# Kernel tuning notes

Hardware: AMD Instinct MI355X
Metric: run time of the kernel (lower is better)

Reference implementation:

```python
import jax, jax.numpy as jnp
import numpy as np

LMAX, MMAX = 4, 2
C_IN, C_OUT = 128, 128           # sphere_channels, m_output_channels
NUM_EXPERTS = 8
NUM_SYSTEMS = 16
NUM_EDGES = 12288
M_SIZE = [LMAX + 1, 2 * (LMAX - 1 + 1), 2 * (LMAX - 2 + 1)]  # [5, 8, 6]


def _mole_linear(x, W, ce, b=None):
    """MoLE linear: per-edge expert mixing of weights, equivalently mixing of
    per-expert outputs.  x: [N, in] or [N, 2, in]; W: [K, in, out]; ce: [N, K]."""
    if x.ndim == 2:
        z = jnp.einsum('ni,kio->nko', x, W)        # [N, K, out]
        y = jnp.einsum('nk,nko->no', ce, z)
    else:
        z = jnp.einsum('nci,kio->nkco', x, W)      # [N, K, 2, out]
        y = jnp.einsum('nk,nkco->nco', ce, z)
    if b is not None:
        y = y + ce @ b                              # mixed bias, b: [K, out]
    return y


def setup_inputs() -> dict:
    key = jax.random.key(0)
    ks = jax.random.split(key, 8)
    num_mcoef = sum(M_SIZE)  # 19
    x = jax.random.normal(ks[0], (NUM_EDGES, num_mcoef, C_IN), dtype=jnp.float32)
    x_edge = jax.random.normal(ks[1], (NUM_EDGES, C_IN), dtype=jnp.float32)
    expert_coefficients = jax.random.uniform(ks[2], (NUM_SYSTEMS, NUM_EXPERTS), dtype=jnp.float32)
    edge_batch = jax.random.randint(ks[3], (NUM_EDGES,), 0, NUM_SYSTEMS)
    # fc_m0: in = (lmax+1)*C, out = (lmax+1)*C_out, with bias
    in0 = (LMAX + 1) * C_IN
    out0 = (LMAX + 1) * C_OUT
    W_m0 = jax.random.normal(ks[4], (NUM_EXPERTS, in0, out0), dtype=jnp.float32) * 0.02
    b_m0 = jnp.zeros((NUM_EXPERTS, out0), dtype=jnp.float32)
    # so2_m_conv m: in = (lmax-m+1)*C, out = 2*(lmax-m+1)*C_out, no bias
    nc1 = LMAX - 1 + 1
    W_m1 = jax.random.normal(ks[5], (NUM_EXPERTS, nc1 * C_IN, 2 * nc1 * C_OUT), dtype=jnp.float32) * 0.02
    nc2 = LMAX - 2 + 1
    W_m2 = jax.random.normal(ks[6], (NUM_EXPERTS, nc2 * C_IN, 2 * nc2 * C_OUT), dtype=jnp.float32) * 0.02
    return {
        'x': x, 'x_edge': x_edge,
        'expert_coefficients': expert_coefficients, 'edge_batch': edge_batch,
        'W_m0': W_m0, 'b_m0': b_m0, 'W_m1': W_m1, 'W_m2': W_m2,
    }


def reference(x, x_edge, expert_coefficients, edge_batch, W_m0, b_m0, W_m1, W_m2):
    N = x.shape[0]
    ce = expert_coefficients[edge_batch]               # [N, K] per-edge mix coeffs
    x0, x1, x2 = jnp.split(x, np.cumsum(M_SIZE[:-1]), axis=1)
    # m = 0 branch (internal_weights=True -> no radial rescale)
    y0 = _mole_linear(x0.reshape(N, -1), W_m0, ce, b_m0)
    out = [y0.reshape(N, -1, C_OUT)]                   # [N, lmax+1, C_out]
    # m >= 1 branches: SO(2) real/imag recombination
    for m, Wm, xm in ((1, W_m1, x1), (2, W_m2, x2)):
        nc = LMAX - m + 1
        xm = xm.reshape(N, 2, nc * C_IN)
        ym = _mole_linear(xm, Wm, ce)                  # [N, 2, 2*nc*C_out]
        ym = ym.reshape(N, 4, nc * C_OUT)
        x_m_r = ym[:, 0] - ym[:, 3]                    # x_r_0 - x_i_1
        x_m_i = ym[:, 2] + ym[:, 1]                    # x_r_1 + x_i_0
        out.append(x_m_r.reshape(N, nc, C_OUT))
        out.append(x_m_i.reshape(N, nc, C_OUT))
    return jnp.concatenate(out, axis=1)                # [N, 19, C_out]
```

## Files before the change

kernel.cpp:

```cpp
#include <hip/hip_runtime.h>
#include <cstdint>

#define N_EDGES 12288
#define ROWLEN  2432
#define CAP     2048

typedef __bf16 bf16;
typedef __bf16 bf16x8 __attribute__((ext_vector_type(8)));
typedef float  f32x4  __attribute__((ext_vector_type(4)));

#define ELEMS0 (640*640)
#define ELEMS1 (1024*1024)
#define ELEMS2 (768*768)

#define WS_IDX_OFF   1024
#define WS_BIAS_OFF  (WS_IDX_OFF + 16*CAP*4)
#define WS_W_OFF     (WS_BIAS_OFF + 16*640*4)
#define WZ_ELEMS     ((size_t)16*(ELEMS0+ELEMS1+ELEMS2))

template<int B> struct Cfg;
template<> struct Cfg<0> { static constexpr int K=640,  KS=640, XOFF=0,    NT=5;
                           static constexpr size_t WOFF=0; };
template<> struct Cfg<1> { static constexpr int K=1024, KS=512, XOFF=640,  NT=8;
                           static constexpr size_t WOFF=(size_t)16*ELEMS0; };
template<> struct Cfg<2> { static constexpr int K=768,  KS=384, XOFF=1664, NT=6;
                           static constexpr size_t WOFF=(size_t)16*ELEMS0+(size_t)16*ELEMS1; };

__device__ __forceinline__ void async_copy16(const void* g, void* l) {
  auto gp = reinterpret_cast<const __attribute__((address_space(1))) unsigned int*>(
      reinterpret_cast<uintptr_t>(g));
  auto lp = reinterpret_cast<__attribute__((address_space(3))) unsigned int*>(
      (unsigned int)reinterpret_cast<uintptr_t>(l));
  __builtin_amdgcn_global_load_lds(gp, lp, 16, 0, 0);
}

__global__ void bucket_kernel(const int* __restrict__ eb, int* __restrict__ counts,
                              int* __restrict__ idxb) {
  __shared__ int hcnt[16], hbase[16];
  int tid = threadIdx.x;
  int t = blockIdx.x * 256 + tid;
  if (tid < 16) hcnt[tid] = 0;
  __syncthreads();
  int s = -1, lp = 0;
  if (t < N_EDGES) { s = eb[t]; lp = atomicAdd(&hcnt[s], 1); }
  __syncthreads();
  if (tid < 16) hbase[tid] = atomicAdd(counts + tid, hcnt[tid]);
  __syncthreads();
  if (s >= 0) { int p = hbase[s] + lp; if (p < CAP) idxb[s * CAP + p] = t; }
}

__global__ void bias_kernel(const float* __restrict__ ce, const float* __restrict__ b0,
                            float* __restrict__ bias) {
  int t = blockIdx.x * 256 + threadIdx.x;
  int s = t / 640, c = t - s * 640;
  float a = 0.f;
#pragma unroll
  for (int e = 0; e < 8; ++e) a += ce[s * 8 + e] * b0[e * 640 + c];
  bias[t] = a;
}

template<int B>
__device__ __forceinline__ void mix_body(const float* __restrict__ Wsrc,
                                         const float* ce_s,
                                         unsigned short* __restrict__ Wz, int pos) {
  constexpr int N = Cfg<B>::K, KS = Cfg<B>::KS, NT = N / 128, HALF = N / 2;
  constexpr int SRC_STRIDE = KS * N;
  constexpr size_t DST_STRIDE = (size_t)Cfg<B>::K * N;
  int nn = pos & 127, kgrp = (pos >> 7) & 3, rest = pos >> 9;
  int nt = rest % NT, kblk = rest / NT;
  int i0 = kblk * 32 + kgrp * 8;
  int c  = nt * 128 + nn;
  int si = i0, sc = c; float sg = 1.f;
  if (B > 0 && i0 >= KS) {
    si = i0 - KS;
    if (c < HALF) { sc = c + HALF; sg = -1.f; } else { sc = c - HALF; }
  }
  float w[8][8];
  const float* p0 = Wsrc + (size_t)si * N + sc;
#pragma unroll
  for (int e = 0; e < 8; ++e) {
    const float* p = p0 + (size_t)e * SRC_STRIDE;
#pragma unroll
    for (int j = 0; j < 8; ++j)
      w[e][j] = sg * __builtin_nontemporal_load(p + (size_t)j * N);
  }
  unsigned short* db = Wz + Cfg<B>::WOFF + (size_t)pos * 8;
#pragma unroll
  for (int s = 0; s < 16; ++s) {
    float a[8] = {0, 0, 0, 0, 0, 0, 0, 0};
#pragma unroll
    for (int e = 0; e < 8; ++e) {
      float cc = ce_s[s * 8 + e];
#pragma unroll
      for (int j = 0; j < 8; ++j) a[j] += cc * w[e][j];
    }
    bf16x8 v;
#pragma unroll
    for (int j = 0; j < 8; ++j) v[j] = (bf16)a[j];
    *(bf16x8*)(db + s * DST_STRIDE) = v;
  }
}

__global__ __launch_bounds__(256) void mix_all(const float* __restrict__ W0,
                                               const float* __restrict__ W1,
                                               const float* __restrict__ W2,
                                               const float* __restrict__ ce,
                                               unsigned short* __restrict__ Wz) {
  __shared__ float ce_s[128];
  int tid = threadIdx.x;
  if (tid < 128) ce_s[tid] = ce[tid];
  __syncthreads();
  int bx = blockIdx.x;
  if (bx < 200)      mix_body<0>(W0, ce_s, Wz, bx * 256 + tid);
  else if (bx < 712) mix_body<1>(W1, ce_s, Wz, (bx - 200) * 256 + tid);
  else               mix_body<2>(W2, ce_s, Wz, (bx - 712) * 256 + tid);
}

template<int B>
__device__ __forceinline__ void gemm_body(
    const float* __restrict__ x, const char* __restrict__ zeros,
    const unsigned short* __restrict__ Wz,
    const int* __restrict__ counts, const int* __restrict__ idxb,
    const float* __restrict__ bias, float* __restrict__ out,
    int s, int mt, int nt2, char* sm, int* eidx)
{
  constexpr int K = Cfg<B>::K, NT = Cfg<B>::NT, KB = K / 32, XOFF = Cfg<B>::XOFF;
  int cnt = counts[s];
  int m0 = mt * 128;
  if (m0 >= cnt) return;
  int tid = threadIdx.x;
  if (tid < 128) eidx[tid] = (m0 + tid < cnt) ? idxb[s * CAP + m0 + tid] : -1;
  __syncthreads();
  char* lA0 = sm;           char* lA1 = sm + 8192;
  char* lB0 = sm + 16384;   char* lB1 = sm + 32768;
  int wv = tid >> 6, ln = tid & 63;
  int wm = wv >> 1, wn = wv & 1;
  int kq = ln >> 4, lm = ln & 15;
  int c0 = nt2 * 2;
  int r_a = tid >> 1, h = tid & 1;
  const char* arow; int kinc;
  { int e = eidx[r_a];
    if (e >= 0) { arow = (const char*)(x + (size_t)e * ROWLEN + XOFF); kinc = 128; }
    else        { arow = zeros; kinc = 0; } }
  const unsigned short* wb = Wz + Cfg<B>::WOFF + (size_t)s * K * K;

  f32x4 sreg[4];
  auto loadA = [&](int kb) {
    const char* p = arow + (size_t)kb * kinc + h * 64;
#pragma unroll
    for (int i = 0; i < 4; ++i) sreg[i] = *(const f32x4*)(p + i * 16);
  };
  auto writeA = [&](char* dst) {
#pragma unroll
    for (int c = 0; c < 2; ++c) {
      bf16x8 v;
#pragma unroll
      for (int j = 0; j < 8; ++j) v[j] = (bf16)sreg[c * 2 + (j >> 2)][j & 3];
      *(bf16x8*)(dst + ((2 * h + c) * 128 + r_a) * 16) = v;
    }
  };
  auto stageB = [&](int kb, char* dst) {
    const unsigned short* base = wb + (size_t)kb * (NT * 4096);
#pragma unroll
    for (int i = 0; i < 4; ++i) {
      int c = i * 256 + tid;
      int ck = c0 + (c >> 9); if (ck > NT - 1) ck = NT - 1;
      async_copy16(base + (size_t)ck * 4096 + (c & 511) * 8,
                   dst + (i * 256 + wv * 64) * 16);
    }
  };

  f32x4 acc[4][8];
#pragma unroll
  for (int i = 0; i < 4; ++i)
#pragma unroll
    for (int j = 0; j < 8; ++j) {
      acc[i][j][0] = 0.f; acc[i][j][1] = 0.f; acc[i][j][2] = 0.f; acc[i][j][3] = 0.f;
    }

  loadA(0); stageB(0, lB0); writeA(lA0);
#pragma unroll 1
  for (int kb = 0; kb < KB; ++kb) {
    __syncthreads();
    char* la = (kb & 1) ? lA1 : lA0;
    char* lb = (kb & 1) ? lB1 : lB0;
    if (kb + 1 < KB) {
      loadA(kb + 1);
      stageB(kb + 1, (kb & 1) ? lB0 : lB1);
    }
    bf16x8 af[4], bq[8];
#pragma unroll
    for (int mi = 0; mi < 4; ++mi)
      af[mi] = *(const bf16x8*)(la + kq * 2048 + (wm * 64 + mi * 16 + lm) * 16);
#pragma unroll
    for (int ni = 0; ni < 8; ++ni)
      bq[ni] = *(const bf16x8*)(lb + wn * 8192 + kq * 2048 + (ni * 16 + lm) * 16);
#pragma unroll
    for (int mi = 0; mi < 4; ++mi)
#pragma unroll
      for (int ni = 0; ni < 8; ++ni)
        acc[mi][ni] = __builtin_amdgcn_mfma_f32_16x16x32_bf16(af[mi], bq[ni], acc[mi][ni], 0, 0, 0);
    if (kb + 1 < KB) writeA((kb & 1) ? lA0 : lA1);
  }
  int cc = c0 + wn;
  if (cc >= NT) return;
  float bv[8] = {0, 0, 0, 0, 0, 0, 0, 0};
  if (B == 0) {
#pragma unroll
    for (int ni = 0; ni < 8; ++ni)
      bv[ni] = bias[s * 640 + cc * 128 + ni * 16 + lm];
  }
#pragma unroll
  for (int mi = 0; mi < 4; ++mi) {
#pragma unroll
    for (int r = 0; r < 4; ++r) {
      int row = wm * 64 + mi * 16 + kq * 4 + r;
      int e = eidx[row];
      if (e < 0) continue;
      float* po = out + (size_t)e * ROWLEN + XOFF + cc * 128 + lm;
#pragma unroll
      for (int ni = 0; ni < 8; ++ni) po[ni * 16] = acc[mi][ni][r] + bv[ni];
    }
  }
}

__global__ __launch_bounds__(256, 2) void gemm_all(
    const float* __restrict__ x, const char* __restrict__ zeros,
    const unsigned short* __restrict__ Wz,
    const int* __restrict__ counts, const int* __restrict__ idxb,
    const float* __restrict__ bias, float* __restrict__ out) {
  extern __shared__ char sm[];
  __shared__ int eidx[128];
  int g = blockIdx.x;
  int xcd = g & 7, j = g >> 3;
  int s = xcd + 8 * (j / 160);
  int r = j % 160;
  int mt = r / 10, bx = r % 10;
  if (bx < 3)      gemm_body<0>(x, zeros, Wz, counts, idxb, bias, out, s, mt, bx,     sm, eidx);
  else if (bx < 7) gemm_body<1>(x, zeros, Wz, counts, idxb, bias, out, s, mt, bx - 3, sm, eidx);
  else             gemm_body<2>(x, zeros, Wz, counts, idxb, bias, out, s, mt, bx - 7, sm, eidx);
}

extern "C" void kernel_launch(void* const* d_in, const int* in_sizes, int n_in,
                              void* d_out, int out_size, void* d_ws, size_t ws_size,
                              hipStream_t stream) {
  const float* x  = (const float*)d_in[0];
  const float* ce = (const float*)d_in[2];
  const int*   eb = (const int*)d_in[3];
  const float* W0 = (const float*)d_in[4];
  const float* b0 = (const float*)d_in[5];
  const float* W1 = (const float*)d_in[6];
  const float* W2 = (const float*)d_in[7];
  float* out = (float*)d_out;
  char* ws = (char*)d_ws;
  int*   counts = (int*)ws;
  char*  zeros  = ws + 256;
  int*   idxb   = (int*)(ws + WS_IDX_OFF);
  float* bias   = (float*)(ws + WS_BIAS_OFF);
  unsigned short* Wz = (unsigned short*)(ws + WS_W_OFF);

  hipMemsetAsync(ws, 0, 1024, stream);
  bucket_kernel<<<48, 256, 0, stream>>>(eb, counts, idxb);
  bias_kernel<<<40, 256, 0, stream>>>(ce, b0, bias);
  mix_all<<<1000, 256, 0, stream>>>(W0, W1, W2, ce, Wz);
  gemm_all<<<2560, 256, 49152, stream>>>(x, zeros, Wz, counts, idxb, bias, out);
}
```

Baseline: 332.0 us.

## Triple-buffer weight tiles with prefetch depth two in MoLE GEMM

The GEMM main loop is reorganised to keep three LDS buffers for the B (mixed weight) tiles, so async weight copies are issued two k-steps ahead. The activation tile stays double-buffered, with its global load issued one step further ahead. The full __syncthreads is replaced by an explicit LDS waitcnt plus s_barrier and sched_barrier, and the MFMA block is bracketed with s_setprio to favour matrix work. The aim is to hide more global-load latency behind MFMA compute. In exchange, dynamic LDS grows from 48KB to 64KB per block, which may cut the number of resident blocks per CU. The correctness of the async-copy completion relies on implicit vmcnt ordering.

Result: no change. 328.6 us (-1.0%).

```diff
diff --git a/kernel.cpp b/kernel.cpp
--- a/kernel.cpp
+++ b/kernel.cpp
@@ -131,8 +131,8 @@
   int tid = threadIdx.x;
   if (tid < 128) eidx[tid] = (m0 + tid < cnt) ? idxb[s * CAP + m0 + tid] : -1;
   __syncthreads();
-  char* lA0 = sm;           char* lA1 = sm + 8192;
-  char* lB0 = sm + 16384;   char* lB1 = sm + 32768;
+  char* Acur = sm;          char* Anxt = sm + 8192;
+  char* Bc = sm + 16384;    char* Bm = sm + 32768;    char* Bn = sm + 49152;
   int wv = tid >> 6, ln = tid & 63;
   int wm = wv >> 1, wn = wv & 1;
   int kq = ln >> 4, lm = ln & 15;
@@ -178,29 +178,42 @@
       acc[i][j][0] = 0.f; acc[i][j][1] = 0.f; acc[i][j][2] = 0.f; acc[i][j][3] = 0.f;
     }
 
-  loadA(0); stageB(0, lB0); writeA(lA0);
+  loadA(0);
+  stageB(0, Bc);
+  writeA(Acur);
+  asm volatile("s_waitcnt vmcnt(0)" ::: "memory");
+  stageB(1, Bm);
+  loadA(1);
+  asm volatile("s_waitcnt lgkmcnt(0)" ::: "memory");
+  __builtin_amdgcn_s_barrier();
+  __builtin_amdgcn_sched_barrier(0);
+
 #pragma unroll 1
   for (int kb = 0; kb < KB; ++kb) {
-    __syncthreads();
-    char* la = (kb & 1) ? lA1 : lA0;
-    char* lb = (kb & 1) ? lB1 : lB0;
-    if (kb + 1 < KB) {
-      loadA(kb + 1);
-      stageB(kb + 1, (kb & 1) ? lB0 : lB1);
-    }
+    if (kb + 2 < KB) stageB(kb + 2, Bn);
     bf16x8 af[4], bq[8];
 #pragma unroll
     for (int mi = 0; mi < 4; ++mi)
-      af[mi] = *(const bf16x8*)(la + kq * 2048 + (wm * 64 + mi * 16 + lm) * 16);
+      af[mi] = *(const bf16x8*)(Acur + kq * 2048 + (wm * 64 + mi * 16 + lm) * 16);
 #pragma unroll
     for (int ni = 0; ni < 8; ++ni)
-      bq[ni] = *(const bf16x8*)(lb + wn * 8192 + kq * 2048 + (ni * 16 + lm) * 16);
+      bq[ni] = *(const bf16x8*)(Bc + wn * 8192 + kq * 2048 + (ni * 16 + lm) * 16);
+    __builtin_amdgcn_s_setprio(1);
 #pragma unroll
     for (int mi = 0; mi < 4; ++mi)
 #pragma unroll
       for (int ni = 0; ni < 8; ++ni)
         acc[mi][ni] = __builtin_amdgcn_mfma_f32_16x16x32_bf16(af[mi], bq[ni], acc[mi][ni], 0, 0, 0);
-    if (kb + 1 < KB) writeA((kb & 1) ? lA0 : lA1);
+    __builtin_amdgcn_s_setprio(0);
+    if (kb + 1 < KB) {
+      writeA(Anxt);
+      if (kb + 2 < KB) loadA(kb + 2);
+    }
+    asm volatile("s_waitcnt lgkmcnt(0)" ::: "memory");
+    __builtin_amdgcn_s_barrier();
+    __builtin_amdgcn_sched_barrier(0);
+    char* t = Acur; Acur = Anxt; Anxt = t;
+    char* tb = Bc; Bc = Bm; Bm = Bn; Bn = tb;
   }
   int cc = c0 + wn;
   if (cc >= NT) return;
@@ -263,5 +276,5 @@
   bucket_kernel<<<48, 256, 0, stream>>>(eb, counts, idxb);
   bias_kernel<<<40, 256, 0, stream>>>(ce, b0, bias);
   mix_all<<<1000, 256, 0, stream>>>(W0, W1, W2, ce, Wz);
-  gemm_all<<<2560, 256, 49152, stream>>>(x, zeros, Wz, counts, idxb, bias, out);
-}
+  gemm_all<<<2560, 256, 65536, stream>>>(x, zeros, Wz, counts, idxb, bias, out);
+}
```
